# Performance work log

Hardware: AMD Instinct MI355X
Metric: run time of the kernel (lower is better)

Reference implementation:

```python
import jax, jax.numpy as jnp
import numpy as np
from jax import lax

K_STEEP = 10.0      # ssm_K: surrogate spike steepness
V_TH_MIN = 0.1      # ssm_v_th_min
EK_FLOOR = 0.01     # ssm_ek_floor


def setup_inputs() -> dict:
    key = jax.random.key(0)
    ks = jax.random.split(key, 11)
    B, T, D, N = 2, 1024, 1024, 16
    s = lambda fan: 1.0 / np.sqrt(fan)
    return {
        "hidden_states": jax.random.normal(ks[0], (B, T, D), jnp.float32),
        "W_xz": jax.random.normal(ks[1], (D, 2 * D), jnp.float32) * s(D),
        "W_dt": jax.random.normal(ks[2], (D, D), jnp.float32) * s(D),
        "b_dt": jax.random.normal(ks[3], (D,), jnp.float32) * 0.1,
        "A_log": jax.random.uniform(ks[4], (D, N), jnp.float32, 0.0, 1.0),
        "W_B": jax.random.normal(ks[5], (D, N), jnp.float32) * s(D),
        "W_C": jax.random.normal(ks[6], (D, N), jnp.float32) * s(D),
        "D_skip": jax.random.normal(ks[7], (D,), jnp.float32) * 0.1,
        "W_out": jax.random.normal(ks[8], (D, D), jnp.float32) * s(D),
        "v_th": jax.random.uniform(ks[9], (D,), jnp.float32, 0.0, 0.5),
    }


def _bio_ssm(h, W_xz, W_dt, b_dt, A_log, W_B, W_C, D_skip, W_out, v_th):
    # h: (T, B, D) time-major, as in the torch wrapper after permute(1,0,2)
    T, B, D = h.shape
    N = A_log.shape[1]
    xz = jnp.einsum('tbd,de->tbe', h, W_xz)
    x, z = jnp.split(xz, 2, axis=-1)                       # (T,B,D) each
    dt = jax.nn.softplus(jnp.einsum('tbd,de->tbe', x, W_dt) + b_dt)  # (T,B,D)
    A = -jnp.exp(A_log)                                     # (D,N), negative
    Bm = jnp.einsum('tbd,dn->tbn', h, W_B)                  # (T,B,N)
    Cm = jnp.einsum('tbd,dn->tbn', h, W_C)                  # (T,B,N)
    decay = jnp.exp(dt[..., None] * A)                      # (T,B,D,N)
    inp = (dt * x)[..., None] * Bm[:, :, None, :]           # (T,B,D,N)

    def step(s, td):
        dec, ip, c = td
        s = dec * s + ip                                    # (B,D,N)
        y = jnp.einsum('bdn,bn->bd', s, c)
        return s, y

    s0 = jnp.zeros((B, D, N), h.dtype)
    _, y = lax.scan(step, s0, (decay, inp, Cm))             # y: (T,B,D)
    y = y + D_skip * x
    vth = jnp.maximum(v_th, V_TH_MIN)
    spike_p = jax.nn.sigmoid(K_STEEP * (y - vth))           # surrogate spiking gate
    y_sp = y * spike_p
    pc = jnp.mean(spike_p)                                  # ponder cost
    efc = jnp.mean(jax.nn.relu(EK_FLOOR - y * y))           # ek-floor cost
    out = jnp.einsum('tbd,de->tbe', y_sp * jax.nn.silu(z), W_out)
    return out, pc, efc


def reference(hidden_states, W_xz, W_dt, b_dt, A_log, W_B, W_C, D_skip, W_out, v_th):
    h = jnp.transpose(hidden_states, (1, 0, 2))             # (T,B,D)
    h_out, pc, efc = _bio_ssm(h, W_xz, W_dt, b_dt, A_log, W_B, W_C, D_skip, W_out, v_th)
    out = h_out - h                                         # mixer residual delta
    return jnp.transpose(out, (1, 0, 2))                    # (B,T,D)
```

## Files before the change

### kernel.cpp

```cpp
#include <hip/hip_runtime.h>
#include <hip/hip_bf16.h>
#include <stdint.h>

#define TT 1024
#define BB 2
#define DD 1024
#define NN 16
#define NCH 256
#define LCH 4

#define K_STEEP 10.0f
#define V_TH_MIN 0.1f
#define L2E 1.44269504088896f

#if defined(__has_builtin)
#if __has_builtin(__builtin_amdgcn_exp2f)
#define EXP2(x) __builtin_amdgcn_exp2f(x)
#endif
#endif
#ifndef EXP2
#define EXP2(x) exp2f(x)
#endif

typedef __bf16 bf16x8 __attribute__((ext_vector_type(8)));
typedef float f32x4 __attribute__((ext_vector_type(4)));

__device__ __forceinline__ short f2bf(float f) {
    union { float f; unsigned u; } c; c.f = f;
    unsigned r = (c.u + 0x7fffu + ((c.u >> 16) & 1u)) >> 16;
    return (short)r;
}
__device__ __forceinline__ float bf2f(short s) {
    union { unsigned u; float f; } c;
    c.u = ((unsigned)(unsigned short)s) << 16;
    return c.f;
}

__device__ __forceinline__ void gload_lds16(const void* g, void* l) {
    __builtin_amdgcn_global_load_lds(
        (const __attribute__((address_space(1))) void*)g,
        (__attribute__((address_space(3))) void*)l, 16, 0, 0);
}

template<int BM, int EPI, bool FUSE_BC>
__global__ __launch_bounds__(256) void gemm_mfma(
    const short* __restrict__ A, int lda,
    const short* __restrict__ BT, int ldb,
    float* __restrict__ C, int ldc,
    int M, int Ncols, int K,
    const float* __restrict__ bias,
    const float* __restrict__ sub,
    short* __restrict__ xb_out,
    short* __restrict__ xzT_out,
    const short* __restrict__ WbcT,
    short* __restrict__ bcs)
{
    constexpr int RI = BM / 32;
    __shared__ short As[BM * 64];
    __shared__ short Bs[128 * 64];

    const int tid = threadIdx.x;
    const int wave = tid >> 6, lane = tid & 63;
    const int kk = (lane >> 4) * 8;
    const int r16 = lane & 15;
    const int wr = wave >> 1, wc = wave & 1;

    if (FUSE_BC && blockIdx.x == gridDim.x - 1) {
        const int bm2 = blockIdx.y * 32;
        f32x4 acc2 = {};
        for (int k0 = 0; k0 < K; k0 += 64) {
            int off = tid * 16;
            int row = off >> 7;
            int ke  = (off & 127) >> 1;
            gload_lds16(A + (size_t)(bm2 + row) * lda + k0 + ke, (char*)As + off);
            gload_lds16(WbcT + (size_t)row * K + k0 + ke, (char*)Bs + off);
            __syncthreads();
            bf16x8 alo = *(const bf16x8*)&As[(wr * 16 + r16) * 64 + kk];
            bf16x8 ahi = *(const bf16x8*)&As[(wr * 16 + r16) * 64 + kk + 32];
            bf16x8 blo = *(const bf16x8*)&Bs[(wc * 16 + r16) * 64 + kk];
            bf16x8 bhi = *(const bf16x8*)&Bs[(wc * 16 + r16) * 64 + kk + 32];
            acc2 = __builtin_amdgcn_mfma_f32_16x16x32_bf16(alo, blo, acc2, 0, 0, 0);
            acc2 = __builtin_amdgcn_mfma_f32_16x16x32_bf16(ahi, bhi, acc2, 0, 0, 0);
            __syncthreads();
        }
        #pragma unroll
        for (int g = 0; g < 4; g++) {
            int row = bm2 + wr * 16 + (lane >> 4) * 4 + g;
            int col = wc * 16 + r16;
            int bb = row >> 10, t = row & 1023;
            int j = t & 3, c = t >> 2;
            bcs[(size_t)(((bb << 2) | j) * NCH + c) * 32 + col] = f2bf(acc2[g]);
        }
        return;
    }

    const int bm = blockIdx.y * BM, bn = blockIdx.x * 128;
    f32x4 acc[RI][4] = {};

    for (int k0 = 0; k0 < K; k0 += 64) {
        #pragma unroll
        for (int it = 0; it < 4; it++) {
            int off = it * 4096 + tid * 16;
            int row = off >> 7;
            int ke  = (off & 127) >> 1;
            gload_lds16(BT + (size_t)(bn + row) * ldb + k0 + ke, (char*)Bs + off);
        }
        if (tid < BM * 8) {
            int off = tid * 16;
            int row = off >> 7;
            int ke  = (off & 127) >> 1;
            gload_lds16(A + (size_t)(bm + row) * lda + k0 + ke, (char*)As + off);
        }
        __syncthreads();

        #pragma unroll
        for (int ks = 0; ks < 64; ks += 32) {
            bf16x8 a[RI], b[4];
            #pragma unroll
            for (int i = 0; i < RI; i++)
                a[i] = *(const bf16x8*)&As[(wr * (BM / 2) + i * 16 + r16) * 64 + ks + kk];
            #pragma unroll
            for (int j = 0; j < 4; j++)
                b[j] = *(const bf16x8*)&Bs[(wc * 64 + j * 16 + r16) * 64 + ks + kk];
            #pragma unroll
            for (int i = 0; i < RI; i++)
                #pragma unroll
                for (int j = 0; j < 4; j++)
                    acc[i][j] = __builtin_amdgcn_mfma_f32_16x16x32_bf16(
                        a[i], b[j], acc[i][j], 0, 0, 0);
        }
        __syncthreads();
    }

    #pragma unroll
    for (int i = 0; i < RI; i++) {
        #pragma unroll
        for (int j = 0; j < 4; j++) {
            int row0 = bm + wr * (BM / 2) + i * 16 + (lane >> 4) * 4;
            int col = bn + wc * 64 + j * 16 + r16;
            if (EPI == 3) {
                short4 p;
                #pragma unroll
                for (int g = 0; g < 4; g++) {
                    short h = f2bf(acc[i][j][g]);
                    ((short*)&p)[g] = h;
                    if (col < DD) xb_out[(size_t)(row0 + g) * DD + col] = h;
                }
                *(short4*)&xzT_out[(size_t)col * 2048 + row0] = p;
            } else {
                #pragma unroll
                for (int g = 0; g < 4; g++) {
                    int row = row0 + g;
                    float v = acc[i][j][g];
                    if (EPI == 4) {
                        v += bias[row];
                        v = fmaxf(v, 0.f) + log1pf(__expf(-fabsf(v)));
                    }
                    if (EPI == 2) {
                        v -= sub[(size_t)row * ldc + col];
                    }
                    C[(size_t)row * ldc + col] = v;
                }
            }
        }
    }
}

__device__ __forceinline__ void tr_tile(
    const float* __restrict__ W, short* __restrict__ WT,
    int K, int N, int k0, int n0, int tid)
{
    __shared__ float t[32][33];
    int r = tid >> 3, q = tid & 7;
    float4 v = *(const float4*)&W[(size_t)(k0 + r) * N + n0 + q * 4];
    t[r][q * 4 + 0] = v.x; t[r][q * 4 + 1] = v.y;
    t[r][q * 4 + 2] = v.z; t[r][q * 4 + 3] = v.w;
    __syncthreads();
    short4 o = { f2bf(t[q * 4 + 0][r]), f2bf(t[q * 4 + 1][r]),
                 f2bf(t[q * 4 + 2][r]), f2bf(t[q * 4 + 3][r]) };
    *(short4*)&WT[(size_t)(n0 + r) * K + k0 + q * 4] = o;
}

__global__ __launch_bounds__(256) void prep_all(
    const float* __restrict__ H,    short* __restrict__ Hb,
    const float* __restrict__ W_xz, short* __restrict__ WxzT,
    const float* __restrict__ W_dt, short* __restrict__ WdtT,
    const float* __restrict__ W_out,short* __restrict__ WoutT,
    const float* __restrict__ W_B,  const float* __restrict__ W_C,
    short* __restrict__ WbcT)
{
    int bid = blockIdx.x, tid = threadIdx.x;
    if (bid < 2048) {
        int i = bid * 1024 + tid * 4;
        float4 v = *(const float4*)&H[i];
        short4 o = { f2bf(v.x), f2bf(v.y), f2bf(v.z), f2bf(v.w) };
        *(short4*)&Hb[i] = o;
    } else if (bid < 4096) {
        int t = bid - 2048;
        tr_tile(W_xz, WxzT, DD, 2 * DD, (t >> 6) * 32, (t & 63) * 32, tid);
    } else if (bid < 5120) {
        int t = bid - 4096;
        tr_tile(W_dt, WdtT, DD, DD, (t >> 5) * 32, (t & 31) * 32, tid);
    } else if (bid < 6144) {
        int t = bid - 5120;
        tr_tile(W_out, WoutT, DD, DD, (t >> 5) * 32, (t & 31) * 32, tid);
    } else {
        int g = (bid - 6144) * 256 + tid;
        int k = g & (DD - 1);
        int n = g >> 10;
        float v = (n < 16) ? W_B[(size_t)k * NN + n]
                           : W_C[(size_t)k * NN + n - 16];
        WbcT[(size_t)n * DD + k] = f2bf(v);
    }
}

__global__ __launch_bounds__(256) void tr_g(
    const short* __restrict__ gT, short* __restrict__ gb)
{
    __shared__ short L[64][72];
    const int bt0 = blockIdx.x * 64, d0 = blockIdx.y * 64;
    const int tid = threadIdx.x;
    const int r = tid >> 3, c8 = (tid & 7) * 8;
    #pragma unroll
    for (int p = 0; p < 2; p++) {
        int dd = r + p * 32;
        *(int4*)&L[dd][c8] = *(const int4*)&gT[(size_t)(d0 + dd) * 2048 + bt0 + c8];
    }
    __syncthreads();
    #pragma unroll
    for (int p = 0; p < 2; p++) {
        int tb = r + p * 32;
        short tmp[8];
        #pragma unroll
        for (int k = 0; k < 8; k++) tmp[k] = L[c8 + k][tb];
        *(int4*)&gb[(size_t)(bt0 + tb) * DD + d0 + c8] = *(int4*)&tmp[0];
    }
}

__global__ __launch_bounds__(512) void scan_fused7(
    const float* __restrict__ dtT,
    const short* __restrict__ xzT,
    const short* __restrict__ bcs,
    const float* __restrict__ A_log,
    const float* __restrict__ D_skip,
    const float* __restrict__ v_th,
    short* __restrict__ gT)
{
    __shared__ float Ls[512 * 17];
    __shared__ float Sd[512];
    __shared__ float Gp[16][2][16];
    __shared__ float Gl[16][2][16];

    const int tid = threadIdx.x;
    const int dl = tid & 1;
    const int c  = tid >> 1;
    const int d  = blockIdx.x * 2 + dl;
    const int b  = blockIdx.y;
    const int R0 = b * TT + c * LCH;

    float a2[NN];
    #pragma unroll
    for (int n = 0; n < NN; n++)
        a2[n] = -__expf(A_log[(size_t)d * NN + n]) * L2E;

    float dtv[LCH];
    *(float4*)&dtv[0] = *(const float4*)&dtT[(size_t)d * 2048 + R0];
    short xv[LCH], zv[LCH];
    *(int2*)&xv[0] = *(const int2*)&xzT[(size_t)d * 2048 + R0];
    *(int2*)&zv[0] = *(const int2*)&xzT[(size_t)(DD + d) * 2048 + R0];

    float s[NN];
    #pragma unroll
    for (int n = 0; n < NN; n++) s[n] = 0.f;
    float sum_dt = 0.f;

    #pragma unroll
    for (int j = 0; j < LCH; j++) {
        float dt = dtv[j];
        float x  = bf2f(xv[j]);
        float dtx = dt * x;
        sum_dt += dt;
        const short* bp = &bcs[(size_t)(((b << 2) | j) * NCH + c) * 32];
        short bB[NN];
        *(int4*)&bB[0] = *(const int4*)&bp[0];
        *(int4*)&bB[8] = *(const int4*)&bp[8];
        #pragma unroll
        for (int n = 0; n < NN; n++) {
            float dec = EXP2(a2[n] * dt);
            s[n] = fmaf(dec, s[n], dtx * bf2f(bB[n]));
        }
    }
    #pragma unroll
    for (int n = 0; n < NN; n++) Ls[tid * 17 + n] = s[n];
    Sd[tid] = sum_dt;
    __syncthreads();

    {
        int dl2 = tid & 1, n2 = (tid >> 1) & 15, sg = tid >> 5;
        float a2n = -__expf(A_log[(size_t)(blockIdx.x * 2 + dl2) * NN + n2]) * L2E;
        float Pg = 1.f, Lg = 0.f;
        for (int k = 0; k < 16; k++) {
            int lt = (sg * 16 + k) * 2 + dl2;
            float P = EXP2(a2n * Sd[lt]);
            float L = Ls[lt * 17 + n2];
            Lg = fmaf(P, Lg, L);
            Pg *= P;
        }
        Gp[sg][dl2][n2] = Pg; Gl[sg][dl2][n2] = Lg;
        __syncthreads();
        if (tid < 32) {
            int dl3 = tid & 1, n3 = tid >> 1;
            float Sg = 0.f;
            for (int g = 0; g < 16; g++) {
                float Pgv = Gp[g][dl3][n3];
                Gp[g][dl3][n3] = Sg;
                Sg = fmaf(Pgv, Sg, Gl[g][dl3][n3]);
            }
        }
        __syncthreads();
        float ss = Gp[sg][dl2][n2];
        for (int k = 0; k < 16; k++) {
            int lt = (sg * 16 + k) * 2 + dl2;
            float P = EXP2(a2n * Sd[lt]);
            float L = Ls[lt * 17 + n2];
            Ls[lt * 17 + n2] = ss;
            ss = fmaf(P, ss, L);
        }
    }
    __syncthreads();

    #pragma unroll
    for (int n = 0; n < NN; n++) s[n] = Ls[tid * 17 + n];

    const float dsk = D_skip[d];
    const float vth = fmaxf(v_th[d], V_TH_MIN);
    const float KL2 = K_STEEP * L2E;
    short gvv[LCH];

    #pragma unroll
    for (int j = 0; j < LCH; j++) {
        float dt = dtv[j];
        float x  = bf2f(xv[j]);
        float z  = bf2f(zv[j]);
        float dtx = dt * x;
        const short* bp = &bcs[(size_t)(((b << 2) | j) * NCH + c) * 32];
        short bB[NN], bC[NN];
        *(int4*)&bB[0] = *(const int4*)&bp[0];
        *(int4*)&bB[8] = *(const int4*)&bp[8];
        *(int4*)&bC[0] = *(const int4*)&bp[16];
        *(int4*)&bC[8] = *(const int4*)&bp[24];
        float y = 0.f;
        #pragma unroll
        for (int n = 0; n < NN; n++) {
            float dec = EXP2(a2[n] * dt);
            s[n] = fmaf(dec, s[n], dtx * bf2f(bB[n]));
            y = fmaf(s[n], bf2f(bC[n]), y);
        }
        y = fmaf(dsk, x, y);
        float sp = 1.f / (1.f + EXP2(-KL2 * (y - vth)));
        float sz = z / (1.f + EXP2(-z * L2E));
        gvv[j] = f2bf(y * sp * sz);
    }

    *(int2*)&gT[(size_t)d * 2048 + R0] = *(const int2*)&gvv[0];
}

extern "C" void kernel_launch(void* const* d_in, const int* in_sizes, int n_in,
                              void* d_out, int out_size, void* d_ws, size_t ws_size,
                              hipStream_t stream) {
    const float* H      = (const float*)d_in[0];
    const float* W_xz   = (const float*)d_in[1];
    const float* W_dt   = (const float*)d_in[2];
    const float* b_dt   = (const float*)d_in[3];
    const float* A_log  = (const float*)d_in[4];
    const float* W_B    = (const float*)d_in[5];
    const float* W_C    = (const float*)d_in[6];
    const float* D_skip = (const float*)d_in[7];
    const float* W_out  = (const float*)d_in[8];
    const float* v_th   = (const float*)d_in[9];
    float* out = (float*)d_out;

    float* ws  = (float*)d_ws;
    float* dtT = ws;
    short* p16   = (short*)(dtT + 2097152);
    short* bcs   = p16;
    short* xzT   = bcs   + 65536;
    short* xb    = xzT   + 4194304;
    short* Hb    = xb    + 2097152;
    short* WxzT  = Hb    + 2097152;
    short* WdtT  = WxzT  + 2097152;
    short* WoutT = WdtT  + 1048576;
    short* WbcT  = WoutT + 1048576;
    short* gT    = WbcT  + 32768;
    short* gb    = gT    + 2097152;

    const int M = BB * TT;

    prep_all<<<6272, 256, 0, stream>>>(
        H, Hb, W_xz, WxzT, W_dt, WdtT, W_out, WoutT, W_B, W_C, WbcT);
    gemm_mfma<32, 3, true><<<dim3(17, M / 32), 256, 0, stream>>>(
        Hb, DD, WxzT, DD, nullptr, 0, M, 2 * DD, DD,
        nullptr, nullptr, xb, xzT, WbcT, bcs);
    gemm_mfma<32, 4, false><<<dim3(M / 128, DD / 32), 256, 0, stream>>>(
        WdtT, DD, xb, DD, dtT, M, DD, M, DD,
        b_dt, nullptr, nullptr, nullptr, nullptr, nullptr);
    scan_fused7<<<dim3(DD / 2, BB), 512, 0, stream>>>(
        dtT, xzT, bcs, A_log, D_skip, v_th, gT);
    tr_g<<<dim3(2048 / 64, DD / 64), 256, 0, stream>>>(gT, gb);
    gemm_mfma<32, 2, false><<<dim3(DD / 128, M / 32), 256, 0, stream>>>(
        gb, DD, WoutT, DD, out, DD, M, DD, DD,
        nullptr, H, nullptr, nullptr, nullptr, nullptr);
}
```

Measured before the change: 104.3 us.

## Store dt as bf16 and reuse local chunk outputs in scan second pass

The dt GEMM epilogue now writes softplus(dt) as bf16 instead of fp32, halving that intermediate's write and read traffic. The scan's first pass also computes the local (zero-initial-state) y contributions and cumulative dt per step. The second pass then adds only the carried-in state's contribution via exp(A*cumdt), so it no longer recomputes the recurrence. This trades extra registers and some precision on dt for less memory traffic and fewer per-step FMAs in the second pass.

```diff
diff --git a/kernel.cpp b/kernel.cpp
--- a/kernel.cpp
+++ b/kernel.cpp
@@ -155,11 +155,11 @@
                     if (EPI == 4) {
                         v += bias[row];
                         v = fmaxf(v, 0.f) + log1pf(__expf(-fabsf(v)));
+                        xb_out[(size_t)row * ldc + col] = f2bf(v);
+                    } else {
+                        if (EPI == 2) v -= sub[(size_t)row * ldc + col];
+                        C[(size_t)row * ldc + col] = v;
                     }
-                    if (EPI == 2) {
-                        v -= sub[(size_t)row * ldc + col];
-                    }
-                    C[(size_t)row * ldc + col] = v;
                 }
             }
         }
@@ -237,8 +237,8 @@
     }
 }
 
-__global__ __launch_bounds__(512) void scan_fused7(
-    const float* __restrict__ dtT,
+__global__ __launch_bounds__(512) void scan_fused8(
+    const short* __restrict__ dtb16,
     const short* __restrict__ xzT,
     const short* __restrict__ bcs,
     const float* __restrict__ A_log,
@@ -263,8 +263,11 @@
     for (int n = 0; n < NN; n++)
         a2[n] = -__expf(A_log[(size_t)d * NN + n]) * L2E;
 
+    short dth[LCH];
+    *(int2*)&dth[0] = *(const int2*)&dtb16[(size_t)d * 2048 + R0];
     float dtv[LCH];
-    *(float4*)&dtv[0] = *(const float4*)&dtT[(size_t)d * 2048 + R0];
+    #pragma unroll
+    for (int j = 0; j < LCH; j++) dtv[j] = bf2f(dth[j]);
     short xv[LCH], zv[LCH];
     *(int2*)&xv[0] = *(const int2*)&xzT[(size_t)d * 2048 + R0];
     *(int2*)&zv[0] = *(const int2*)&xzT[(size_t)(DD + d) * 2048 + R0];
@@ -273,22 +276,28 @@
     #pragma unroll
     for (int n = 0; n < NN; n++) s[n] = 0.f;
     float sum_dt = 0.f;
+    float cdt[LCH], yloc[LCH];
 
     #pragma unroll
     for (int j = 0; j < LCH; j++) {
         float dt = dtv[j];
-        float x  = bf2f(xv[j]);
-        float dtx = dt * x;
+        float dtx = dt * bf2f(xv[j]);
         sum_dt += dt;
+        cdt[j] = sum_dt;
         const short* bp = &bcs[(size_t)(((b << 2) | j) * NCH + c) * 32];
-        short bB[NN];
+        short bB[NN], bC[NN];
         *(int4*)&bB[0] = *(const int4*)&bp[0];
         *(int4*)&bB[8] = *(const int4*)&bp[8];
+        *(int4*)&bC[0] = *(const int4*)&bp[16];
+        *(int4*)&bC[8] = *(const int4*)&bp[24];
+        float y = 0.f;
         #pragma unroll
         for (int n = 0; n < NN; n++) {
             float dec = EXP2(a2[n] * dt);
             s[n] = fmaf(dec, s[n], dtx * bf2f(bB[n]));
-        }
+            y = fmaf(s[n], bf2f(bC[n]), y);
+        }
+        yloc[j] = y;
     }
     #pragma unroll
     for (int n = 0; n < NN; n++) Ls[tid * 17 + n] = s[n];
@@ -339,23 +348,18 @@
 
     #pragma unroll
     for (int j = 0; j < LCH; j++) {
-        float dt = dtv[j];
-        float x  = bf2f(xv[j]);
-        float z  = bf2f(zv[j]);
-        float dtx = dt * x;
         const short* bp = &bcs[(size_t)(((b << 2) | j) * NCH + c) * 32];
-        short bB[NN], bC[NN];
-        *(int4*)&bB[0] = *(const int4*)&bp[0];
-        *(int4*)&bB[8] = *(const int4*)&bp[8];
+        short bC[NN];
         *(int4*)&bC[0] = *(const int4*)&bp[16];
         *(int4*)&bC[8] = *(const int4*)&bp[24];
-        float y = 0.f;
+        float y = yloc[j];
         #pragma unroll
         for (int n = 0; n < NN; n++) {
-            float dec = EXP2(a2[n] * dt);
-            s[n] = fmaf(dec, s[n], dtx * bf2f(bB[n]));
-            y = fmaf(s[n], bf2f(bC[n]), y);
-        }
+            float e = EXP2(a2[n] * cdt[j]);
+            y = fmaf(bf2f(bC[n]) * e, s[n], y);
+        }
+        float x = bf2f(xv[j]);
+        float z = bf2f(zv[j]);
         y = fmaf(dsk, x, y);
         float sp = 1.f / (1.f + EXP2(-KL2 * (y - vth)));
         float sz = z / (1.f + EXP2(-z * L2E));
@@ -380,10 +384,9 @@
     const float* v_th   = (const float*)d_in[9];
     float* out = (float*)d_out;
 
-    float* ws  = (float*)d_ws;
-    float* dtT = ws;
-    short* p16   = (short*)(dtT + 2097152);
-    short* bcs   = p16;
+    short* p16   = (short*)d_ws;
+    short* dtb16 = p16;
+    short* bcs   = dtb16 + 2097152;
     short* xzT   = bcs   + 65536;
     short* xb    = xzT   + 4194304;
     short* Hb    = xb    + 2097152;
@@ -402,10 +405,10 @@
         Hb, DD, WxzT, DD, nullptr, 0, M, 2 * DD, DD,
         nullptr, nullptr, xb, xzT, WbcT, bcs);
     gemm_mfma<32, 4, false><<<dim3(M / 128, DD / 32), 256, 0, stream>>>(
-        WdtT, DD, xb, DD, dtT, M, DD, M, DD,
-        b_dt, nullptr, nullptr, nullptr, nullptr, nullptr);
-    scan_fused7<<<dim3(DD / 2, BB), 512, 0, stream>>>(
-        dtT, xzT, bcs, A_log, D_skip, v_th, gT);
+        WdtT, DD, xb, DD, nullptr, M, DD, M, DD,
+        b_dt, nullptr, dtb16, nullptr, nullptr, nullptr);
+    scan_fused8<<<dim3(DD / 2, BB), 512, 0, stream>>>(
+        dtb16, xzT, bcs, A_log, D_skip, v_th, gT);
     tr_g<<<dim3(2048 / 64, DD / 64), 256, 0, stream>>>(gT, gb);
     gemm_mfma<32, 2, false><<<dim3(DD / 128, M / 32), 256, 0, stream>>>(
         gb, DD, WoutT, DD, out, DD, M, DD, DD,
```

Measured after the change: 108.7 us. 4.3% more time.
